# Performance work log

Hardware: AMD Instinct MI355X
Metric: run time of the kernel (lower is better)

The kernel has to match this reference:

```python
import math
import jax, jax.numpy as jnp
import numpy as np

HIDDEN = 768
N_SIGNALS = 15
DIM = HIDDEN // 4  # 192
B, S = 32, 4096


def setup_inputs() -> dict:
    key = jax.random.key(0)
    ks = jax.random.split(key, 11)
    return {
        "token_embeds": jax.random.normal(ks[0], (B, S, HIDDEN), jnp.float32),
        "Wk": jax.random.normal(ks[1], (HIDDEN, DIM), jnp.float32) * 0.02,
        "bk": jax.random.normal(ks[2], (DIM,), jnp.float32) * 0.02,
        "Wv": jax.random.normal(ks[3], (HIDDEN, DIM), jnp.float32) * 0.02,
        "bv": jax.random.normal(ks[4], (DIM,), jnp.float32) * 0.02,
        "signal_queries": jax.random.normal(ks[5], (N_SIGNALS, DIM), jnp.float32),
        "null_embeddings": jax.random.normal(ks[6], (N_SIGNALS, HIDDEN), jnp.float32) * 0.01,
        "W1": jax.random.normal(ks[7], (2 * DIM, 64), jnp.float32) * 0.05,
        "b1": jax.random.normal(ks[8], (64,), jnp.float32) * 0.05,
        "W2": jax.random.normal(ks[9], (64, 1), jnp.float32) * 0.05,
        "b2": jax.random.normal(ks[10], (1,), jnp.float32) * 0.05,
    }


def reference(token_embeds, Wk, bk, Wv, bv, signal_queries, null_embeddings, W1, b1, W2, b2):
    b, s, h = token_embeds.shape
    d = Wk.shape[1]
    # detect_signals: cross-attention from signal queries to tokens
    keys = token_embeds @ Wk + bk        # [B,S,d]
    values = token_embeds @ Wv + bv      # [B,S,d]
    scale = jnp.sqrt(jnp.float32(d))
    attn = jnp.einsum("nd,bsd->bns", signal_queries, keys) / scale  # [B,N,S]
    attn_weights = jax.nn.softmax(attn, axis=-1)
    signal_embeds = jnp.einsum("bns,bsd->bnd", attn_weights, values)  # [B,N,d]
    entropy = -(attn_weights * jnp.log(attn_weights + 1e-10)).sum(-1)  # [B,N]
    strength = 1.0 - entropy / jnp.float32(math.log(s))
    # estimate_causal_effects: batched over the 15 signals (original loops in Python)
    null_proj = jnp.broadcast_to(null_embeddings[:, :d], (b, null_embeddings.shape[0], d))
    eff_in = jnp.concatenate([signal_embeds, null_proj], axis=-1)  # [B,N,2d]
    hdn = jax.nn.gelu(eff_in @ W1 + b1, approximate=False)
    effects = (hdn @ W2 + b2)[..., 0]  # [B,N]
    # package (effects, strength) as one array [B, 2N]
    return jnp.concatenate([effects, strength], axis=-1)
```

## Files before the change

### kernel.cpp

```cpp
#include <hip/hip_runtime.h>
#include <math.h>

#define HID   768
#define DIMD  192
#define NSIG  15
#define BB    32
#define SS    4096
#define SC    128
#define NCHUNK (SS / SC)
#define HC    32
#define NHC   (384 / HC)
#define INV_SCALE 0.07216878364870322f
#define LOG_S     8.31776616671934f

#define WS_QK   ((size_t)0)
#define WS_QB   (WS_QK + NSIG * HID)
#define WS_ST   (WS_QB + 16)
#define WS_CTXP (WS_ST + (size_t)BB * NCHUNK * NSIG * 3)

__global__ __launch_bounds__(256) void k_qk(const float* __restrict__ q,
                                            const float* __restrict__ Wk,
                                            const float* __restrict__ bk,
                                            float* __restrict__ ws) {
  int idx = blockIdx.x * 256 + threadIdx.x;
  if (idx < NSIG * HID) {
    int n = idx / HID, h = idx - n * HID;
    const float* qr = q + n * DIMD;
    const float* wr = Wk + h * DIMD;
    float s = 0.f;
    #pragma unroll 4
    for (int d = 0; d < DIMD; ++d) s = fmaf(qr[d], wr[d], s);
    ws[WS_QK + (size_t)n * HID + h] = s * INV_SCALE;
  }
  if (idx < NSIG) {
    const float* qr = q + idx * DIMD;
    float s = 0.f;
    for (int d = 0; d < DIMD; ++d) s = fmaf(qr[d], bk[d], s);
    ws[WS_QB + idx] = s * INV_SCALE;
  }
}

__global__ __launch_bounds__(256, 4) void k_fused(const float* __restrict__ X,
                                                  const float* __restrict__ qk,
                                                  const float* __restrict__ qb,
                                                  float* __restrict__ stats,
                                                  float* __restrict__ ctxp) {
  __shared__ float smem[2 * SC * 33];
  const int t = threadIdx.x;
  const int chunk = blockIdx.x, b = blockIdx.y;
  const int tk = t & (SC - 1);
  const int hf = __builtin_amdgcn_readfirstlane(t >> 7);
  const float* Xb = X + ((size_t)(b * SS + chunk * SC)) * HID;

  float4 r[8];
  #pragma unroll
  for (int k = 0; k < 8; ++k) {
    int j = t + k * 256;
    int c4 = j & 7, row = (j >> 3) & (SC - 1), half = j >> 10;
    r[k] = *(const float4*)(Xb + (size_t)row * HID + half * 384 + c4 * 4);
  }

  float acc[NSIG];
  #pragma unroll
  for (int n = 0; n < NSIG; ++n) acc[n] = (hf == 0) ? qb[n] : 0.f;

  for (int c = 0; c < NHC; ++c) {
    __syncthreads();
    #pragma unroll
    for (int k = 0; k < 8; ++k) {
      int j = t + k * 256;
      int c4 = j & 7, row = (j >> 3) & (SC - 1), half = j >> 10;
      float* dst = smem + (half * SC + row) * 33 + c4 * 4;
      dst[0] = r[k].x; dst[1] = r[k].y; dst[2] = r[k].z; dst[3] = r[k].w;
    }
    __syncthreads();
    if (c + 1 < NHC) {
      #pragma unroll
      for (int k = 0; k < 8; ++k) {
        int j = t + k * 256;
        int c4 = j & 7, row = (j >> 3) & (SC - 1), half = j >> 10;
        r[k] = *(const float4*)(Xb + (size_t)row * HID + half * 384 + (c + 1) * HC + c4 * 4);
      }
    }
    const float* xrow = smem + (hf * SC + tk) * 33;
    float x[HC];
    #pragma unroll
    for (int j = 0; j < HC; ++j) x[j] = xrow[j];
    const float* Qc = qk + hf * 384 + c * HC;
    #pragma unroll
    for (int n = 0; n < NSIG; ++n) {
      const float* Qn = Qc + (size_t)n * HID;
      float s = 0.f;
      #pragma unroll
      for (int j = 0; j < HC; ++j) s = fmaf(x[j], Qn[j], s);
      acc[n] += s;
    }
  }

  __syncthreads();
  float* comb = smem;
  float* wS   = smem + NSIG * SC;
  float* redM = smem + 2 * NSIG * SC;
  float* redL = redM + NSIG * 2;
  float* redP = redL + NSIG * 2;
  const int wv = __builtin_amdgcn_readfirstlane(t >> 6);

  if (hf == 1) {
    #pragma unroll
    for (int n = 0; n < NSIG; ++n) comb[n * SC + tk] = acc[n];
  }
  __syncthreads();
  if (hf == 0) {
    #pragma unroll
    for (int n = 0; n < NSIG; ++n) {
      acc[n] += comb[n * SC + tk];
      float v = acc[n];
      #pragma unroll
      for (int o = 32; o > 0; o >>= 1) v = fmaxf(v, __shfl_xor(v, o, 64));
      if ((t & 63) == 0) redM[n * 2 + wv] = v;
    }
  }
  __syncthreads();
  if (hf == 0) {
    #pragma unroll
    for (int n = 0; n < NSIG; ++n) {
      float m = fmaxf(redM[n * 2], redM[n * 2 + 1]);
      float e = expf(acc[n] - m);
      wS[n * SC + tk] = e;
      float l = e, pa = e * acc[n];
      #pragma unroll
      for (int o = 32; o > 0; o >>= 1) { l += __shfl_xor(l, o, 64); pa += __shfl_xor(pa, o, 64); }
      if ((t & 63) == 0) { redL[n * 2 + wv] = l; redP[n * 2 + wv] = pa; }
    }
  }
  __syncthreads();
  if (t < NSIG) {
    float m  = fmaxf(redM[t * 2], redM[t * 2 + 1]);
    float l  = redL[t * 2] + redL[t * 2 + 1];
    float pa = redP[t * 2] + redP[t * 2 + 1];
    float* st = stats + ((size_t)((b * NCHUNK + chunk) * NSIG + t)) * 3;
    st[0] = m; st[1] = l; st[2] = pa;
  }

  float accB[NSIG * 3];
  #pragma unroll
  for (int i = 0; i < NSIG * 3; ++i) accB[i] = 0.f;
  const float* Xc = Xb + t;
  for (int s = 0; s < SC; s += 4) {
    float x[12];
    #pragma unroll
    for (int j = 0; j < 4; ++j)
      #pragma unroll
      for (int k = 0; k < 3; ++k)
        x[j * 3 + k] = Xc[(size_t)(s + j) * HID + k * 256];
    #pragma unroll
    for (int n = 0; n < NSIG; ++n) {
      float4 w4 = *(const float4*)(wS + n * SC + s);
      float wa[4] = {w4.x, w4.y, w4.z, w4.w};
      #pragma unroll
      for (int j = 0; j < 4; ++j)
        #pragma unroll
        for (int k = 0; k < 3; ++k)
          accB[n * 3 + k] = fmaf(wa[j], x[j * 3 + k], accB[n * 3 + k]);
    }
  }
  float* dst = ctxp + ((size_t)((b * NCHUNK + chunk) * NSIG)) * HID + t;
  #pragma unroll
  for (int n = 0; n < NSIG; ++n)
    #pragma unroll
    for (int k = 0; k < 3; ++k)
      dst[(size_t)n * HID + k * 256] = accB[n * 3 + k];
}

__global__ __launch_bounds__(256) void k_final(const float* __restrict__ stats,
                                               const float* __restrict__ ctxp,
                                               const float* __restrict__ Wv,
                                               const float* __restrict__ bv,
                                               const float* __restrict__ nullemb,
                                               const float* __restrict__ W1,
                                               const float* __restrict__ b1,
                                               const float* __restrict__ W2,
                                               const float* __restrict__ b2,
                                               float* __restrict__ out) {
  const int blk = blockIdx.x;
  const int b = blk / NSIG, n = blk - b * NSIG;
  const int t = threadIdx.x;
  __shared__ float alpha[NCHUNK];
  __shared__ float ctx[HID];
  __shared__ float se[DIMD];

  if (t == 0) {
    float mc[NCHUNK], lc[NCHUNK], pc[NCHUNK];
    float m = -1e30f;
    #pragma unroll
    for (int c = 0; c < NCHUNK; ++c) {
      const float* st = stats + ((size_t)((b * NCHUNK + c) * NSIG + n)) * 3;
      mc[c] = st[0]; lc[c] = st[1]; pc[c] = st[2];
      m = fmaxf(m, mc[c]);
    }
    float L = 0.f, PA = 0.f;
    #pragma unroll
    for (int c = 0; c < NCHUNK; ++c) {
      float scl = expf(mc[c] - m);
      L = fmaf(scl, lc[c], L); PA = fmaf(scl, pc[c], PA);
    }
    #pragma unroll
    for (int c = 0; c < NCHUNK; ++c) alpha[c] = expf(mc[c] - m) / L;
    float entropy = m + logf(L) - PA / L;
    out[b * (2 * NSIG) + NSIG + n] = 1.f - entropy / LOG_S;
  }
  __syncthreads();

  #pragma unroll
  for (int k = 0; k < 3; ++k) {
    int h = t + k * 256;
    float s = 0.f;
    #pragma unroll 8
    for (int c = 0; c < NCHUNK; ++c)
      s = fmaf(alpha[c], ctxp[((size_t)((b * NCHUNK + c) * NSIG + n)) * HID + h], s);
    ctx[h] = s;
  }
  __syncthreads();

  if (t < DIMD) {
    float s = bv[t];
    #pragma unroll 4
    for (int h = 0; h < HID; ++h)
      s = fmaf(ctx[h], Wv[(size_t)h * DIMD + t], s);
    se[t] = s;
  }
  __syncthreads();

  if (t < 64) {
    float s = b1[t];
    const float* nrow = nullemb + (size_t)n * HID;
    #pragma unroll 4
    for (int i = 0; i < DIMD; ++i) s = fmaf(se[i],   W1[(size_t)i * 64 + t], s);
    #pragma unroll 4
    for (int i = 0; i < DIMD; ++i) s = fmaf(nrow[i], W1[(size_t)(DIMD + i) * 64 + t], s);
    float g = 0.5f * s * (1.f + erff(s * 0.70710678118654752f));
    float val = g * W2[t];
    #pragma unroll
    for (int o = 32; o > 0; o >>= 1) val += __shfl_down(val, o, 64);
    if (t == 0) out[b * (2 * NSIG) + n] = val + b2[0];
  }
}

extern "C" void kernel_launch(void* const* d_in, const int* in_sizes, int n_in,
                              void* d_out, int out_size, void* d_ws, size_t ws_size,
                              hipStream_t stream) {
  const float* X   = (const float*)d_in[0];
  const float* Wk  = (const float*)d_in[1];
  const float* bk  = (const float*)d_in[2];
  const float* Wv  = (const float*)d_in[3];
  const float* bv  = (const float*)d_in[4];
  const float* q   = (const float*)d_in[5];
  const float* nul = (const float*)d_in[6];
  const float* W1  = (const float*)d_in[7];
  const float* b1  = (const float*)d_in[8];
  const float* W2  = (const float*)d_in[9];
  const float* b2  = (const float*)d_in[10];
  float* out = (float*)d_out;
  float* ws  = (float*)d_ws;

  hipLaunchKernelGGL(k_qk, dim3(45), dim3(256), 0, stream, q, Wk, bk, ws);
  hipLaunchKernelGGL(k_fused, dim3(NCHUNK, BB), dim3(256), 0, stream,
                     X, ws + WS_QK, ws + WS_QB, ws + WS_ST, ws + WS_CTXP);
  hipLaunchKernelGGL(k_final, dim3(BB * NSIG), dim3(256), 0, stream,
                     ws + WS_ST, ws + WS_CTXP, Wv, bv, nul, W1, b1, W2, b2, out);
}
```

Baseline: 820.7 us.

## Widen fused attention block to 512 threads splitting hidden into quarters and signals

The fused score/context kernel moves from 256 to 512 threads per block. Scores are now computed over four 192-wide quarters of the hidden dimension and combined through shared memory, and the weighted-sum phase splits the 15 signals across two thread halves (8 each, with a zero-padded 16th row). The final kernel's reductions are split into several independent accumulators to shorten FMA dependency chains. Per-thread register pressure drops and more waves are in flight to hide memory latency, at the cost of extra shared-memory combining and one idle signal slot.

```diff
diff --git a/kernel.cpp b/kernel.cpp
--- a/kernel.cpp
+++ b/kernel.cpp
@@ -8,8 +8,8 @@
 #define SS    4096
 #define SC    128
 #define NCHUNK (SS / SC)
-#define HC    32
-#define NHC   (384 / HC)
+#define HC2   16
+#define NST   (192 / HC2)
 #define INV_SCALE 0.07216878364870322f
 #define LOG_S     8.31776616671934f
 
@@ -40,80 +40,81 @@
   }
 }
 
-__global__ __launch_bounds__(256, 4) void k_fused(const float* __restrict__ X,
+__global__ __launch_bounds__(512, 8) void k_fused(const float* __restrict__ X,
                                                   const float* __restrict__ qk,
                                                   const float* __restrict__ qb,
                                                   float* __restrict__ stats,
                                                   float* __restrict__ ctxp) {
-  __shared__ float smem[2 * SC * 33];
+  __shared__ float smem[4 * SC * 17];
   const int t = threadIdx.x;
   const int chunk = blockIdx.x, b = blockIdx.y;
   const int tk = t & (SC - 1);
-  const int hf = __builtin_amdgcn_readfirstlane(t >> 7);
+  const int q  = __builtin_amdgcn_readfirstlane(t >> 7);
   const float* Xb = X + ((size_t)(b * SS + chunk * SC)) * HID;
 
-  float4 r[8];
-  #pragma unroll
-  for (int k = 0; k < 8; ++k) {
-    int j = t + k * 256;
-    int c4 = j & 7, row = (j >> 3) & (SC - 1), half = j >> 10;
-    r[k] = *(const float4*)(Xb + (size_t)row * HID + half * 384 + c4 * 4);
+  float4 r[4];
+  #pragma unroll
+  for (int m = 0; m < 4; ++m) {
+    int j = t + m * 512;
+    int c4 = j & 3, row = (j >> 2) & (SC - 1), qq = j >> 9;
+    r[m] = *(const float4*)(Xb + (size_t)row * HID + qq * DIMD + c4 * 4);
   }
 
   float acc[NSIG];
   #pragma unroll
-  for (int n = 0; n < NSIG; ++n) acc[n] = (hf == 0) ? qb[n] : 0.f;
-
-  for (int c = 0; c < NHC; ++c) {
+  for (int n = 0; n < NSIG; ++n) acc[n] = (q == 0) ? qb[n] : 0.f;
+
+  for (int c = 0; c < NST; ++c) {
     __syncthreads();
     #pragma unroll
-    for (int k = 0; k < 8; ++k) {
-      int j = t + k * 256;
-      int c4 = j & 7, row = (j >> 3) & (SC - 1), half = j >> 10;
-      float* dst = smem + (half * SC + row) * 33 + c4 * 4;
-      dst[0] = r[k].x; dst[1] = r[k].y; dst[2] = r[k].z; dst[3] = r[k].w;
+    for (int m = 0; m < 4; ++m) {
+      int j = t + m * 512;
+      int c4 = j & 3, row = (j >> 2) & (SC - 1), qq = j >> 9;
+      float* dst = smem + (qq * SC + row) * 17 + c4 * 4;
+      dst[0] = r[m].x; dst[1] = r[m].y; dst[2] = r[m].z; dst[3] = r[m].w;
     }
     __syncthreads();
-    if (c + 1 < NHC) {
-      #pragma unroll
-      for (int k = 0; k < 8; ++k) {
-        int j = t + k * 256;
-        int c4 = j & 7, row = (j >> 3) & (SC - 1), half = j >> 10;
-        r[k] = *(const float4*)(Xb + (size_t)row * HID + half * 384 + (c + 1) * HC + c4 * 4);
+    if (c + 1 < NST) {
+      #pragma unroll
+      for (int m = 0; m < 4; ++m) {
+        int j = t + m * 512;
+        int c4 = j & 3, row = (j >> 2) & (SC - 1), qq = j >> 9;
+        r[m] = *(const float4*)(Xb + (size_t)row * HID + qq * DIMD + (c + 1) * HC2 + c4 * 4);
       }
     }
-    const float* xrow = smem + (hf * SC + tk) * 33;
-    float x[HC];
-    #pragma unroll
-    for (int j = 0; j < HC; ++j) x[j] = xrow[j];
-    const float* Qc = qk + hf * 384 + c * HC;
+    const float* xrow = smem + (q * SC + tk) * 17;
+    float x[HC2];
+    #pragma unroll
+    for (int j = 0; j < HC2; ++j) x[j] = xrow[j];
+    const float* Qc = qk + q * DIMD + c * HC2;
     #pragma unroll
     for (int n = 0; n < NSIG; ++n) {
       const float* Qn = Qc + (size_t)n * HID;
       float s = 0.f;
       #pragma unroll
-      for (int j = 0; j < HC; ++j) s = fmaf(x[j], Qn[j], s);
+      for (int j = 0; j < HC2; ++j) s = fmaf(x[j], Qn[j], s);
       acc[n] += s;
     }
   }
 
   __syncthreads();
   float* comb = smem;
-  float* wS   = smem + NSIG * SC;
-  float* redM = smem + 2 * NSIG * SC;
+  float* redM = smem + 3 * NSIG * SC;
   float* redL = redM + NSIG * 2;
   float* redP = redL + NSIG * 2;
-  const int wv = __builtin_amdgcn_readfirstlane(t >> 6);
-
-  if (hf == 1) {
-    #pragma unroll
-    for (int n = 0; n < NSIG; ++n) comb[n * SC + tk] = acc[n];
-  }
-  __syncthreads();
-  if (hf == 0) {
+  float* wS   = smem + 3 * NSIG * SC + 96;
+  const int wv = __builtin_amdgcn_readfirstlane((t >> 6) & 1);
+
+  if (q != 0) {
+    #pragma unroll
+    for (int n = 0; n < NSIG; ++n) comb[((q - 1) * NSIG + n) * SC + tk] = acc[n];
+  }
+  if (t >= 384) wS[NSIG * SC + (t - 384)] = 0.f;
+  __syncthreads();
+  if (q == 0) {
     #pragma unroll
     for (int n = 0; n < NSIG; ++n) {
-      acc[n] += comb[n * SC + tk];
+      acc[n] += comb[n * SC + tk] + comb[(NSIG + n) * SC + tk] + comb[(2 * NSIG + n) * SC + tk];
       float v = acc[n];
       #pragma unroll
       for (int o = 32; o > 0; o >>= 1) v = fmaxf(v, __shfl_xor(v, o, 64));
@@ -121,7 +122,7 @@
     }
   }
   __syncthreads();
-  if (hf == 0) {
+  if (q == 0) {
     #pragma unroll
     for (int n = 0; n < NSIG; ++n) {
       float m = fmaxf(redM[n * 2], redM[n * 2 + 1]);
@@ -142,10 +143,13 @@
     st[0] = m; st[1] = l; st[2] = pa;
   }
 
-  float accB[NSIG * 3];
-  #pragma unroll
-  for (int i = 0; i < NSIG * 3; ++i) accB[i] = 0.f;
-  const float* Xc = Xb + t;
+  const int cc = t & 255;
+  const int nh = __builtin_amdgcn_readfirstlane(t >> 8);
+  const int n0 = nh * 8;
+  float accB[24];
+  #pragma unroll
+  for (int i = 0; i < 24; ++i) accB[i] = 0.f;
+  const float* Xc = Xb + cc;
   for (int s = 0; s < SC; s += 4) {
     float x[12];
     #pragma unroll
@@ -154,22 +158,23 @@
       for (int k = 0; k < 3; ++k)
         x[j * 3 + k] = Xc[(size_t)(s + j) * HID + k * 256];
     #pragma unroll
-    for (int n = 0; n < NSIG; ++n) {
-      float4 w4 = *(const float4*)(wS + n * SC + s);
+    for (int i = 0; i < 8; ++i) {
+      float4 w4 = *(const float4*)(wS + (n0 + i) * SC + s);
       float wa[4] = {w4.x, w4.y, w4.z, w4.w};
       #pragma unroll
       for (int j = 0; j < 4; ++j)
         #pragma unroll
         for (int k = 0; k < 3; ++k)
-          accB[n * 3 + k] = fmaf(wa[j], x[j * 3 + k], accB[n * 3 + k]);
-    }
-  }
-  float* dst = ctxp + ((size_t)((b * NCHUNK + chunk) * NSIG)) * HID + t;
-  #pragma unroll
-  for (int n = 0; n < NSIG; ++n)
-    #pragma unroll
-    for (int k = 0; k < 3; ++k)
-      dst[(size_t)n * HID + k * 256] = accB[n * 3 + k];
+          accB[i * 3 + k] = fmaf(wa[j], x[j * 3 + k], accB[i * 3 + k]);
+    }
+  }
+  float* dst = ctxp + ((size_t)((b * NCHUNK + chunk) * NSIG)) * HID + cc;
+  #pragma unroll
+  for (int i = 0; i < 8; ++i)
+    if (n0 + i < NSIG)
+      #pragma unroll
+      for (int k = 0; k < 3; ++k)
+        dst[(size_t)(n0 + i) * HID + k * 256] = accB[i * 3 + k];
 }
 
 __global__ __launch_bounds__(256) void k_final(const float* __restrict__ stats,
@@ -214,30 +219,43 @@
   #pragma unroll
   for (int k = 0; k < 3; ++k) {
     int h = t + k * 256;
-    float s = 0.f;
+    float s0 = 0.f, s1 = 0.f;
     #pragma unroll 8
-    for (int c = 0; c < NCHUNK; ++c)
-      s = fmaf(alpha[c], ctxp[((size_t)((b * NCHUNK + c) * NSIG + n)) * HID + h], s);
-    ctx[h] = s;
+    for (int c = 0; c < NCHUNK; c += 2) {
+      s0 = fmaf(alpha[c],     ctxp[((size_t)((b * NCHUNK + c)     * NSIG + n)) * HID + h], s0);
+      s1 = fmaf(alpha[c + 1], ctxp[((size_t)((b * NCHUNK + c + 1) * NSIG + n)) * HID + h], s1);
+    }
+    ctx[h] = s0 + s1;
   }
   __syncthreads();
 
   if (t < DIMD) {
-    float s = bv[t];
-    #pragma unroll 4
-    for (int h = 0; h < HID; ++h)
-      s = fmaf(ctx[h], Wv[(size_t)h * DIMD + t], s);
-    se[t] = s;
+    float s0 = 0.f, s1 = 0.f, s2 = 0.f, s3 = 0.f;
+    #pragma unroll 2
+    for (int h = 0; h < HID; h += 4) {
+      s0 = fmaf(ctx[h],     Wv[(size_t)h       * DIMD + t], s0);
+      s1 = fmaf(ctx[h + 1], Wv[(size_t)(h + 1) * DIMD + t], s1);
+      s2 = fmaf(ctx[h + 2], Wv[(size_t)(h + 2) * DIMD + t], s2);
+      s3 = fmaf(ctx[h + 3], Wv[(size_t)(h + 3) * DIMD + t], s3);
+    }
+    se[t] = bv[t] + ((s0 + s1) + (s2 + s3));
   }
   __syncthreads();
 
   if (t < 64) {
-    float s = b1[t];
+    float s0 = b1[t], s1 = 0.f, s2 = 0.f, s3 = 0.f;
     const float* nrow = nullemb + (size_t)n * HID;
     #pragma unroll 4
-    for (int i = 0; i < DIMD; ++i) s = fmaf(se[i],   W1[(size_t)i * 64 + t], s);
+    for (int i = 0; i < DIMD; i += 2) {
+      s0 = fmaf(se[i],     W1[(size_t)i       * 64 + t], s0);
+      s1 = fmaf(se[i + 1], W1[(size_t)(i + 1) * 64 + t], s1);
+    }
     #pragma unroll 4
-    for (int i = 0; i < DIMD; ++i) s = fmaf(nrow[i], W1[(size_t)(DIMD + i) * 64 + t], s);
+    for (int i = 0; i < DIMD; i += 2) {
+      s2 = fmaf(nrow[i],     W1[(size_t)(DIMD + i)     * 64 + t], s2);
+      s3 = fmaf(nrow[i + 1], W1[(size_t)(DIMD + i + 1) * 64 + t], s3);
+    }
+    float s = (s0 + s1) + (s2 + s3);
     float g = 0.5f * s * (1.f + erff(s * 0.70710678118654752f));
     float val = g * W2[t];
     #pragma unroll
@@ -264,7 +282,7 @@
   float* ws  = (float*)d_ws;
 
   hipLaunchKernelGGL(k_qk, dim3(45), dim3(256), 0, stream, q, Wk, bk, ws);
-  hipLaunchKernelGGL(k_fused, dim3(NCHUNK, BB), dim3(256), 0, stream,
+  hipLaunchKernelGGL(k_fused, dim3(NCHUNK, BB), dim3(512), 0, stream,
                      X, ws + WS_QK, ws + WS_QB, ws + WS_ST, ws + WS_CTXP);
   hipLaunchKernelGGL(k_final, dim3(BB * NSIG), dim3(256), 0, stream,
                      ws + WS_ST, ws + WS_CTXP, Wv, bv, nul, W1, b1, W2, b2, out);
```

New measurement: 736.0 us. 1.12x faster.
